# Performance work log

Measured on AMD Instinct MI355X. Metric: run time of the kernel, lower is better.

The kernel has to match this reference:

```python
import jax, jax.numpy as jnp
import numpy as np

B = 2_000_000
EPS = 1e-7


def _skew(v):
    # v: [..., 3] -> [..., 3, 3] skew-symmetric
    z = jnp.zeros_like(v[..., 0])
    return jnp.stack([
        jnp.stack([z, -v[..., 2], v[..., 1]], axis=-1),
        jnp.stack([v[..., 2], z, -v[..., 0]], axis=-1),
        jnp.stack([-v[..., 1], v[..., 0], z], axis=-1),
    ], axis=-2)


def _rodrigues(phi):
    # axis-angle [..., 3] -> rotation matrix [..., 3, 3]
    angle = jnp.linalg.norm(phi, axis=-1, keepdims=True)
    axis = phi / jnp.maximum(angle, 1e-12)
    K = _skew(axis)
    a = angle[..., None]
    I = jnp.eye(3, dtype=phi.dtype)
    return I + jnp.sin(a) * K + (1.0 - jnp.cos(a)) * (K @ K)


def setup_inputs() -> dict:
    key = jax.random.key(0)
    k1, k2, k3 = jax.random.split(key, 3)
    # random rotations via exp-map of random axis-angle vectors
    phi_est = jax.random.normal(k1, (B, 3), dtype=jnp.float32) * 0.8
    phi_tgt = jax.random.normal(k2, (B, 3), dtype=jnp.float32) * 0.8
    C_est = _rodrigues(phi_est)
    C_target = _rodrigues(phi_tgt)
    # SPD information matrices: A A^T + I  (logdet well-defined)
    A = 0.3 * jax.random.normal(k3, (B, 3, 3), dtype=jnp.float32)
    Rinv = jnp.einsum('bij,bkj->bik', A, A) + jnp.eye(3, dtype=jnp.float32)
    return {"C_est": C_est, "C_target": C_target, "Rinv": Rinv}


def so3_log(C):
    # batched SO(3) log map -> [..., 3]
    tr = C[..., 0, 0] + C[..., 1, 1] + C[..., 2, 2]
    cos_angle = jnp.clip(0.5 * (tr - 1.0), -1.0 + EPS, 1.0 - EPS)
    angle = jnp.arccos(cos_angle)
    sin_angle = jnp.sin(angle)
    # angle/(2 sin angle); small-angle Taylor: 0.5 + angle^2/12
    small = angle < 1e-6
    coef = jnp.where(small, 0.5 + angle * angle / 12.0,
                     0.5 * angle / jnp.where(small, 1.0, sin_angle))
    skew = C - jnp.swapaxes(C, -1, -2)
    vee = jnp.stack([skew[..., 2, 1], skew[..., 0, 2], skew[..., 1, 0]], axis=-1)
    return coef[..., None] * vee


def batch_logdet3(M):
    det = (M[..., 0, 0] * (M[..., 1, 1] * M[..., 2, 2] - M[..., 1, 2] * M[..., 2, 1])
           - M[..., 0, 1] * (M[..., 1, 0] * M[..., 2, 2] - M[..., 1, 2] * M[..., 2, 0])
           + M[..., 0, 2] * (M[..., 1, 0] * M[..., 2, 1] - M[..., 1, 1] * M[..., 2, 0]))
    return jnp.log(det)


def reference(C_est, C_target, Rinv):
    # residual = log(C_est @ C_target^T)  -> [B, 3]
    dC = jnp.einsum('bij,bkj->bik', C_est, C_target)
    residual = so3_log(dC)
    # 0.5 * r^T Rinv r  -> [B]
    weighted = 0.5 * jnp.einsum('bi,bij,bj->b', residual, Rinv, residual)
    nll = weighted - 0.5 * batch_logdet3(Rinv)
    return nll
```

## Files before the change

kernel.cpp:

```cpp
#include <hip/hip_runtime.h>

constexpr int BLK = 256;

__device__ __forceinline__ float mul_rn(float a, float b) {
    float r; asm("v_mul_f32 %0, %1, %2" : "=v"(r) : "v"(a), "v"(b)); return r;
}
__device__ __forceinline__ float add_rn(float a, float b) {
    float r; asm("v_add_f32 %0, %1, %2" : "=v"(r) : "v"(a), "v"(b)); return r;
}
__device__ __forceinline__ float sub_rn(float a, float b) {
    float r; asm("v_sub_f32 %0, %1, %2" : "=v"(r) : "v"(a), "v"(b)); return r;
}
__device__ __forceinline__ float fma_rn(float a, float b, float c) {
    float r; asm("v_fma_f32 %0, %1, %2, %3"
                 : "=v"(r) : "v"(a), "v"(b), "v"(c)); return r;
}

__device__ __forceinline__ float dot3_fma_asc(float a0, float a1, float a2,
                                              float b0, float b1, float b2) {
    return fma_rn(a2, b2, fma_rn(a1, b1, mul_rn(a0, b0)));
}

__global__ __launch_bounds__(BLK) void so3_nll_kernel(
    const float* __restrict__ C_est,
    const float* __restrict__ C_tgt,
    const float* __restrict__ Rinv,
    float* __restrict__ out,
    int B)
{
    __shared__ float sE[BLK * 9];
    __shared__ float sT[BLK * 9];
    __shared__ float sR[BLK * 9];

    const int tid  = threadIdx.x;
    const int b0   = blockIdx.x * BLK;
    const int nrem = min(BLK, B - b0);
    const int nflt = nrem * 9;
    const int nvec = nflt >> 2;

    const float4* gE = reinterpret_cast<const float4*>(C_est + (size_t)b0 * 9);
    const float4* gT = reinterpret_cast<const float4*>(C_tgt + (size_t)b0 * 9);
    const float4* gR = reinterpret_cast<const float4*>(Rinv  + (size_t)b0 * 9);

    for (int i = tid; i < nvec; i += BLK) {
        float4 e = gE[i];
        float4 t = gT[i];
        float4 r = gR[i];
        *reinterpret_cast<float4*>(&sE[i * 4]) = e;
        *reinterpret_cast<float4*>(&sT[i * 4]) = t;
        *reinterpret_cast<float4*>(&sR[i * 4]) = r;
    }
    for (int i = (nvec << 2) + tid; i < nflt; i += BLK) {
        sE[i] = C_est[(size_t)b0 * 9 + i];
        sT[i] = C_tgt[(size_t)b0 * 9 + i];
        sR[i] = Rinv [(size_t)b0 * 9 + i];
    }
    __syncthreads();

    if (tid < nrem) {
        const float* E = &sE[tid * 9];
        const float* T = &sT[tid * 9];
        const float* R = &sR[tid * 9];

        float d00 = dot3_fma_asc(E[0],E[1],E[2], T[0],T[1],T[2]);
        float d11 = dot3_fma_asc(E[3],E[4],E[5], T[3],T[4],T[5]);
        float d22 = dot3_fma_asc(E[6],E[7],E[8], T[6],T[7],T[8]);

        float tr = add_rn(add_rn(d00, d11), d22);
        float ca = 0.5f * sub_rn(tr, 1.0f);
        constexpr float HI = 1.0f - 1e-7f;
        ca = fminf(fmaxf(ca, -HI), HI);
        float angle = acosf(ca);
        float sa    = sinf(angle);
        float coef = (0.5f * angle) / sa;

        float d01 = dot3_fma_asc(E[0],E[1],E[2], T[3],T[4],T[5]);
        float d02 = dot3_fma_asc(E[0],E[1],E[2], T[6],T[7],T[8]);
        float d10 = dot3_fma_asc(E[3],E[4],E[5], T[0],T[1],T[2]);
        float d12 = dot3_fma_asc(E[3],E[4],E[5], T[6],T[7],T[8]);
        float d20 = dot3_fma_asc(E[6],E[7],E[8], T[0],T[1],T[2]);
        float d21 = dot3_fma_asc(E[6],E[7],E[8], T[3],T[4],T[5]);

        float r0 = coef * sub_rn(d21, d12);
        float r1 = coef * sub_rn(d02, d20);
        float r2 = coef * sub_rn(d10, d01);

        float w = 0.5f * (r0 * ((R[0]*r0 + R[1]*r1) + R[2]*r2) +
                          r1 * ((R[3]*r0 + R[4]*r1) + R[5]*r2) +
                          r2 * ((R[6]*r0 + R[7]*r1) + R[8]*r2));

        float det = R[0] * (R[4]*R[8] - R[5]*R[7])
                  - R[1] * (R[3]*R[8] - R[5]*R[6])
                  + R[2] * (R[3]*R[7] - R[4]*R[6]);

        out[b0 + tid] = w - 0.5f * logf(det);
    }
}

extern "C" void kernel_launch(void* const* d_in, const int* in_sizes, int n_in,
                              void* d_out, int out_size, void* d_ws, size_t ws_size,
                              hipStream_t stream) {
    const float* C_est = (const float*)d_in[0];
    const float* C_tgt = (const float*)d_in[1];
    const float* Rinv  = (const float*)d_in[2];
    float* out = (float*)d_out;

    const int B = in_sizes[0] / 9;
    const int blocks = (B + BLK - 1) / BLK;
    so3_nll_kernel<<<blocks, BLK, 0, stream>>>(C_est, C_tgt, Rinv, out, B);
}
```

Measured before the change: 207.3 us.

## Load per-thread 3x3 matrices directly from global, drop LDS staging

```diff
diff --git a/kernel.cpp b/kernel.cpp
--- a/kernel.cpp
+++ b/kernel.cpp
@@ -21,80 +21,65 @@
     return fma_rn(a2, b2, fma_rn(a1, b1, mul_rn(a0, b0)));
 }
 
-__global__ __launch_bounds__(BLK) void so3_nll_kernel(
+__device__ __forceinline__ void load9(const float* __restrict__ p, float* d) {
+    float4 a, b;
+    __builtin_memcpy(&a, p,     16);
+    __builtin_memcpy(&b, p + 4, 16);
+    float c = p[8];
+    d[0] = a.x; d[1] = a.y; d[2] = a.z; d[3] = a.w;
+    d[4] = b.x; d[5] = b.y; d[6] = b.z; d[7] = b.w;
+    d[8] = c;
+}
+
+__global__ __launch_bounds__(BLK, 8) void so3_nll_kernel(
     const float* __restrict__ C_est,
     const float* __restrict__ C_tgt,
     const float* __restrict__ Rinv,
     float* __restrict__ out,
     int B)
 {
-    __shared__ float sE[BLK * 9];
-    __shared__ float sT[BLK * 9];
-    __shared__ float sR[BLK * 9];
+    const int i_raw = blockIdx.x * BLK + threadIdx.x;
+    const int i     = min(i_raw, B - 1);
+    const size_t base = (size_t)i * 9;
 
-    const int tid  = threadIdx.x;
-    const int b0   = blockIdx.x * BLK;
-    const int nrem = min(BLK, B - b0);
-    const int nflt = nrem * 9;
-    const int nvec = nflt >> 2;
+    float E[9], T[9], R[9];
+    load9(C_est + base, E);
+    load9(C_tgt + base, T);
+    load9(Rinv  + base, R);
 
-    const float4* gE = reinterpret_cast<const float4*>(C_est + (size_t)b0 * 9);
-    const float4* gT = reinterpret_cast<const float4*>(C_tgt + (size_t)b0 * 9);
-    const float4* gR = reinterpret_cast<const float4*>(Rinv  + (size_t)b0 * 9);
+    float d00 = dot3_fma_asc(E[0],E[1],E[2], T[0],T[1],T[2]);
+    float d11 = dot3_fma_asc(E[3],E[4],E[5], T[3],T[4],T[5]);
+    float d22 = dot3_fma_asc(E[6],E[7],E[8], T[6],T[7],T[8]);
 
-    for (int i = tid; i < nvec; i += BLK) {
-        float4 e = gE[i];
-        float4 t = gT[i];
-        float4 r = gR[i];
-        *reinterpret_cast<float4*>(&sE[i * 4]) = e;
-        *reinterpret_cast<float4*>(&sT[i * 4]) = t;
-        *reinterpret_cast<float4*>(&sR[i * 4]) = r;
-    }
-    for (int i = (nvec << 2) + tid; i < nflt; i += BLK) {
-        sE[i] = C_est[(size_t)b0 * 9 + i];
-        sT[i] = C_tgt[(size_t)b0 * 9 + i];
-        sR[i] = Rinv [(size_t)b0 * 9 + i];
-    }
-    __syncthreads();
+    float tr = add_rn(add_rn(d00, d11), d22);
+    float ca = 0.5f * sub_rn(tr, 1.0f);
+    constexpr float HI = 1.0f - 1e-7f;
+    ca = fminf(fmaxf(ca, -HI), HI);
+    float angle = acosf(ca);
+    float sa    = sinf(angle);
+    float coef = (0.5f * angle) / sa;
 
-    if (tid < nrem) {
-        const float* E = &sE[tid * 9];
-        const float* T = &sT[tid * 9];
-        const float* R = &sR[tid * 9];
+    float d01 = dot3_fma_asc(E[0],E[1],E[2], T[3],T[4],T[5]);
+    float d02 = dot3_fma_asc(E[0],E[1],E[2], T[6],T[7],T[8]);
+    float d10 = dot3_fma_asc(E[3],E[4],E[5], T[0],T[1],T[2]);
+    float d12 = dot3_fma_asc(E[3],E[4],E[5], T[6],T[7],T[8]);
+    float d20 = dot3_fma_asc(E[6],E[7],E[8], T[0],T[1],T[2]);
+    float d21 = dot3_fma_asc(E[6],E[7],E[8], T[3],T[4],T[5]);
 
-        float d00 = dot3_fma_asc(E[0],E[1],E[2], T[0],T[1],T[2]);
-        float d11 = dot3_fma_asc(E[3],E[4],E[5], T[3],T[4],T[5]);
-        float d22 = dot3_fma_asc(E[6],E[7],E[8], T[6],T[7],T[8]);
+    float r0 = coef * sub_rn(d21, d12);
+    float r1 = coef * sub_rn(d02, d20);
+    float r2 = coef * sub_rn(d10, d01);
 
-        float tr = add_rn(add_rn(d00, d11), d22);
-        float ca = 0.5f * sub_rn(tr, 1.0f);
-        constexpr float HI = 1.0f - 1e-7f;
-        ca = fminf(fmaxf(ca, -HI), HI);
-        float angle = acosf(ca);
-        float sa    = sinf(angle);
-        float coef = (0.5f * angle) / sa;
+    float w = 0.5f * (r0 * ((R[0]*r0 + R[1]*r1) + R[2]*r2) +
+                      r1 * ((R[3]*r0 + R[4]*r1) + R[5]*r2) +
+                      r2 * ((R[6]*r0 + R[7]*r1) + R[8]*r2));
 
-        float d01 = dot3_fma_asc(E[0],E[1],E[2], T[3],T[4],T[5]);
-        float d02 = dot3_fma_asc(E[0],E[1],E[2], T[6],T[7],T[8]);
-        float d10 = dot3_fma_asc(E[3],E[4],E[5], T[0],T[1],T[2]);
-        float d12 = dot3_fma_asc(E[3],E[4],E[5], T[6],T[7],T[8]);
-        float d20 = dot3_fma_asc(E[6],E[7],E[8], T[0],T[1],T[2]);
-        float d21 = dot3_fma_asc(E[6],E[7],E[8], T[3],T[4],T[5]);
+    float det = R[0] * (R[4]*R[8] - R[5]*R[7])
+              - R[1] * (R[3]*R[8] - R[5]*R[6])
+              + R[2] * (R[3]*R[7] - R[4]*R[6]);
 
-        float r0 = coef * sub_rn(d21, d12);
-        float r1 = coef * sub_rn(d02, d20);
-        float r2 = coef * sub_rn(d10, d01);
-
-        float w = 0.5f * (r0 * ((R[0]*r0 + R[1]*r1) + R[2]*r2) +
-                          r1 * ((R[3]*r0 + R[4]*r1) + R[5]*r2) +
-                          r2 * ((R[6]*r0 + R[7]*r1) + R[8]*r2));
-
-        float det = R[0] * (R[4]*R[8] - R[5]*R[7])
-                  - R[1] * (R[3]*R[8] - R[5]*R[6])
-                  + R[2] * (R[3]*R[7] - R[4]*R[6]);
-
-        out[b0 + tid] = w - 0.5f * logf(det);
-    }
+    if (i_raw < B)
+        out[i_raw] = w - 0.5f * logf(det);
 }
 
 extern "C" void kernel_launch(void* const* d_in, const int* in_sizes, int n_in,
```

Measured after the change: 206.5 us. Within noise of the previous version (-0.4%).
